# Optimization experiments

Measured on AMD Instinct MI355X. Metric: run time of the kernel, lower is better.

## Reference

```python
import jax, jax.numpy as jnp
import numpy as np

B, T, M, F, H, O = 64, 168, 256, 32, 128, 32
TWO_OVER_PI = 2.0 / np.pi


def setup_inputs() -> dict:
    key = jax.random.key(0)
    ks = jax.random.split(key, 8)
    return {
        "x": jax.random.normal(ks[0], (B, T, M, F), dtype=jnp.float32),
        "assoc_W": jax.random.normal(ks[1], (F, M, M), dtype=jnp.float32) * (1.0 / np.sqrt(M)),
        "W_ih": jax.random.normal(ks[2], (4 * H, F), dtype=jnp.float32) * (1.0 / np.sqrt(F)),
        "W_hh": jax.random.normal(ks[3], (4 * H, H), dtype=jnp.float32) * (1.0 / np.sqrt(H)),
        "b_ih": jax.random.normal(ks[4], (4 * H,), dtype=jnp.float32) * 0.01,
        "b_hh": jax.random.normal(ks[5], (4 * H,), dtype=jnp.float32) * 0.01,
        "dense_W": jax.random.normal(ks[6], (O, H), dtype=jnp.float32) * (1.0 / np.sqrt(H)),
        "dense_b": jax.random.normal(ks[7], (O,), dtype=jnp.float32) * 0.01,
    }


def _forward(x, assoc_W, W_ih, W_hh, b_ih, b_hh, dense_W, dense_b):
    # x: [B, T, M, F] (batch_first) -> scan over time
    xt = jnp.transpose(x, (1, 0, 2, 3))  # [T, B, M, F]
    b, m = x.shape[0], x.shape[2]
    h0 = jnp.zeros((b, m, H), dtype=x.dtype)
    c0 = jnp.zeros((b, m, H), dtype=x.dtype)

    def step(carry, xin):
        h, c = carry
        # ArcTanNorm: squash into (-1, 1)
        y = jnp.arctan(xin) * TWO_OVER_PI                      # [B, M, F]
        # ICFA: per-attribute association across map units
        y = jnp.einsum('amn,bna->bma', assoc_W, y)             # [B, M, F]
        # LSTM cell (shared weights across map units), PyTorch gate order i,f,g,o
        gates = (jnp.einsum('bmf,gf->bmg', y, W_ih) + b_ih
                 + jnp.einsum('bmh,gh->bmg', h, W_hh) + b_hh)  # [B, M, 4H]
        i, f, g, o = jnp.split(gates, 4, axis=-1)
        i, f, o = jax.nn.sigmoid(i), jax.nn.sigmoid(f), jax.nn.sigmoid(o)
        g = jnp.tanh(g)
        c = f * c + i * g
        h = o * jnp.tanh(c)
        # Dense output head
        out = jnp.einsum('bmh,oh->bmo', h, dense_W) + dense_b  # [B, M, O]
        return (h, c), out

    _, outs = jax.lax.scan(step, (h0, c0), xt)                 # [T, B, M, O]
    return jnp.transpose(outs, (1, 0, 2, 3))                   # [B, T, M, O]


def reference(x, assoc_W, W_ih, W_hh, b_ih, b_hh, dense_W, dense_b):
    return _forward(x, assoc_W, W_ih, W_hh, b_ih, b_hh, dense_W, dense_b)
```

## Files before the change

kernel.cpp:

```cpp
#include <hip/hip_runtime.h>

#define B_  64
#define T_  168
#define M_  256
#define F_  32
#define H_  128
#define O_  32
#define BT_ (B_*T_)

typedef __attribute__((ext_vector_type(8))) short bh8;
typedef __attribute__((ext_vector_type(4))) short sh4;
typedef __attribute__((ext_vector_type(4))) float fx4;

static __device__ __forceinline__ short f2bf(float f) {
  unsigned u = __float_as_uint(f);
  u += 0x7FFFu + ((u >> 16) & 1u);
  return (short)(u >> 16);
}
static __device__ __forceinline__ unsigned cvtpk(float lo, float hi) {
  unsigned r;
  asm("v_cvt_pk_bf16_f32 %0, %1, %2" : "=v"(r) : "v"(lo), "v"(hi));
  return r;
}
static __device__ __forceinline__ float ex2_(float x) {
#if __has_builtin(__builtin_amdgcn_exp2f)
  return __builtin_amdgcn_exp2f(x);
#else
  return exp2f(x);
#endif
}
static __device__ __forceinline__ float rcp_(float x) {
#if __has_builtin(__builtin_amdgcn_rcpf)
  return __builtin_amdgcn_rcpf(x);
#else
  return 1.0f / x;
#endif
}
static __device__ __forceinline__ float sigm(float x) {
  return 1.0f / (1.0f + __expf(-x));
}
static __device__ __forceinline__ float tanh_f(float x) {
  return 1.0f - 2.0f / (1.0f + __expf(2.0f * x));
}
static __device__ __forceinline__ fx4 mm16(bh8 a, bh8 b, fx4 c) {
  return __builtin_amdgcn_mfma_f32_16x16x32_bf16(a, b, c, 0, 0, 0);
}
static __device__ __forceinline__ bh8 cvt8(fx4 p0, fx4 p1) {
  bh8 s;
  s[0] = f2bf(p0[0]); s[1] = f2bf(p0[1]); s[2] = f2bf(p0[2]); s[3] = f2bf(p0[3]);
  s[4] = f2bf(p1[0]); s[5] = f2bf(p1[1]); s[6] = f2bf(p1[2]); s[7] = f2bf(p1[3]);
  return s;
}


__global__ __launch_bounds__(512) void atan_tr(const float* __restrict__ x,
                                               short* __restrict__ ut) {
  __shared__ __align__(16) short tl[8 * 32 * 68];
  const int tid = threadIdx.x;
  const float c2p = 0.63661977236758134f;
  for (int it = 0; it < 21; ++it) {
    const int id = blockIdx.x + it * 256;
    const int bt0 = (id >> 2) * 8, n0 = (id & 3) * 64;
    if (it) __syncthreads();
#pragma unroll
    for (int i = 0; i < 8; ++i) {
      int idx = tid + i * 512;
      int aq = idx & 7, nl = (idx >> 3) & 63, btl = idx >> 9;
      const float* src = x + (long)(bt0 + btl) * 8192 + (n0 + nl) * 32 + aq * 4;
      fx4 v = *(const fx4*)src;
      int base = (btl * 32 + aq * 4) * 68 + nl;
#pragma unroll
      for (int k = 0; k < 4; ++k)
        tl[base + k * 68] = f2bf(atanf(v[k]) * c2p);
    }
    __syncthreads();
#pragma unroll
    for (int p = 0; p < 8; ++p) {
      int r = p * 32 + (tid >> 4);
      int a = r >> 3, btl = r & 7, nq = tid & 15;
      sh4 v = *(const sh4*)&tl[(btl * 32 + a) * 68 + nq * 4];
      *(sh4*)&ut[((long)a * BT_ + bt0 + btl) * 256 + n0 + nq * 4] = v;
    }
  }
}

__global__ __launch_bounds__(512) void icfa_gemm(const short* __restrict__ ut,
                                                 const float* __restrict__ aw,
                                                 short* __restrict__ y) {
  __shared__ __align__(16) short waf[8 * 8 * 64 * 8];
  __shared__ __align__(16) short ubf[64 * 256];
  const int tid = threadIdx.x;
  const int lane = tid & 63, w = tid >> 6, l15 = lane & 15, l4 = lane >> 4;
  const int a = blockIdx.x >> 3, s = blockIdx.x & 7;
  const long ua = (long)a * BT_;

  for (int mh = 0; mh < 2; ++mh) {
    __syncthreads();
    for (int i = 0; i < 8; ++i) {
      int idx = tid + i * 512;
      int ln = idx & 63, ks = (idx >> 6) & 7, mt = idx >> 9;
      const float* src = aw + a * 65536 + (mh * 128 + mt * 16 + (ln & 15)) * 256
                         + ks * 32 + (ln >> 4) * 8;
      *(bh8*)&waf[idx * 8] = cvt8(*(const fx4*)src, *(const fx4*)(src + 4));
    }
    __syncthreads();
    bh8 Af[8];
#pragma unroll
    for (int ks = 0; ks < 8; ++ks)
      Af[ks] = *(const bh8*)&waf[((w * 8 + ks) * 64 + lane) * 8];

    for (int tile = 0; tile < 21; ++tile) {
      const int bt0 = s * 1344 + tile * 64;
      __syncthreads();
#pragma unroll
      for (int i = 0; i < 4; ++i) {
        int idx = tid + i * 512;
        int row = idx >> 5, slot = idx & 31;
        bh8 v = *(const bh8*)&ut[(ua + bt0 + row) * 256 + slot * 8];
        int sb = (row * 512 + slot * 16) ^ ((row & 7) << 4);
        *(bh8*)&((char*)ubf)[sb] = v;
      }
      __syncthreads();
#pragma unroll
      for (int ct = 0; ct < 4; ++ct) {
        fx4 acc = {0.f, 0.f, 0.f, 0.f};
        const int btr = ct * 16 + l15;
#pragma unroll
        for (int ks = 0; ks < 8; ++ks) {
          int byo = (btr * 512 + ks * 64 + l4 * 16) ^ ((btr & 7) << 4);
          bh8 Bf = *(const bh8*)&((char*)ubf)[byo];
          acc = mm16(Af[ks], Bf, acc);
        }
        sh4 o;
        o[0] = f2bf(acc[0]); o[1] = f2bf(acc[1]);
        o[2] = f2bf(acc[2]); o[3] = f2bf(acc[3]);
        *(sh4*)&y[(ua + bt0 + btr) * 256 + mh * 128 + w * 16 + l4 * 4] = o;
      }
    }
  }
}

__global__ __launch_bounds__(512, 2) void lstm_fused8(
    const short* __restrict__ y,
    const float* __restrict__ Wih, const float* __restrict__ Whh,
    const float* __restrict__ bih, const float* __restrict__ bhh,
    const float* __restrict__ dW,  const float* __restrict__ db,
    float* __restrict__ out) {
  __shared__ __align__(16) short hx[8704];
  __shared__ __align__(16) short ytr[2048];
  const int tid = threadIdx.x;
  const int lane = tid & 63, wg = tid >> 6, l15 = lane & 15, l4 = lane >> 4;
  const int bidx = blockIdx.x >> 2, m0 = (blockIdx.x & 3) * 64;
  const float L2E = 1.4426950408889634f;

  for (int i = 0; i < 9; ++i) {
    int j = tid + i * 512;
    if (j < 4352) ((int*)hx)[j] = 0;
  }
  bh8 wrg[4][4];
#pragma unroll
  for (int g = 0; g < 4; ++g)
#pragma unroll
    for (int ks = 0; ks < 4; ++ks) {
      const float* src = Whh + ((g * 8 + wg) * 16 + l15) * 128 + ks * 32 + l4 * 8;
      wrg[g][ks] = cvt8(*(const fx4*)src, *(const fx4*)(src + 4));
    }

  bh8 wfih[4]; float nb[4][4];
#pragma unroll
  for (int gate = 0; gate < 4; ++gate) {
    int grow = (gate * 8 + wg) * 16;
    const float* src = Wih + (grow + l15) * 32 + l4 * 8;
    wfih[gate] = cvt8(*(const fx4*)src, *(const fx4*)(src + 4));
#pragma unroll
    for (int r = 0; r < 4; ++r) {
      int g = grow + l4 * 4 + r;
      float b = bih[g] + bhh[g];
      nb[gate][r] = (gate == 2) ? (2.0f * L2E * b) : (-L2E * b);
    }
  }
  bh8 df[4]; float dbv[4];
  const int oc = wg >> 2, mt_d = wg & 3;
#pragma unroll
  for (int ks = 0; ks < 4; ++ks) {
    const float* src = dW + (oc * 16 + l15) * 128 + ks * 32 + l4 * 8;
    df[ks] = cvt8(*(const fx4*)src, *(const fx4*)(src + 4));
  }
#pragma unroll
  for (int r = 0; r < 4; ++r) dbv[r] = db[oc * 16 + l4 * 4 + r];

  float cst[4][4];
#pragma unroll
  for (int mt = 0; mt < 4; ++mt)
#pragma unroll
    for (int r = 0; r < 4; ++r) cst[mt][r] = 0.f;

  char* hxc = (char*)hx;
  const int hrb = l15 * 272 + l4 * 16;
  const int hdb = (mt_d * 16 + l15) * 272 + l4 * 16;
  const int hwb = l15 * 272 + wg * 32 + l4 * 8;
  const int ar = tid >> 4, mq = tid & 15;
  const long yrow = (long)ar * BT_ + (long)bidx * T_;
  const int ytre = ((mq >> 2) * 64 + ((ar >> 3) << 4) + (mq & 3) * 4) * 8 + (ar & 7);
  const long obB = (long)bidx * T_ * 8192
                 + (long)(m0 + mt_d * 16 + l15) * 32 + oc * 16 + l4 * 4;

  sh4 ys = *(const sh4*)&y[(yrow + 0) * 256 + m0 + mq * 4];
#pragma unroll
  for (int j = 0; j < 4; ++j) ytr[ytre + j * 8] = ys[j];
  ys = *(const sh4*)&y[(yrow + 1) * 256 + m0 + mq * 4];
  __syncthreads();

  for (int t = 0; t < T_; ++t) {
    sh4 ysn = {0, 0, 0, 0};
    if (t + 2 < T_) ysn = *(const sh4*)&y[(yrow + t + 2) * 256 + m0 + mq * 4];
    fx4 acc[4][4];
    {
      bh8 yB[4];
#pragma unroll
      for (int mt = 0; mt < 4; ++mt)
        yB[mt] = *(const bh8*)&ytr[(mt * 64 + lane) * 8];
      fx4 Z = {0.f, 0.f, 0.f, 0.f};
#pragma unroll
      for (int g = 0; g < 4; ++g)
#pragma unroll
        for (int mt = 0; mt < 4; ++mt)
          acc[g][mt] = mm16(wfih[g], yB[mt], Z);
    }
#pragma unroll
    for (int ks = 0; ks < 4; ++ks) {
      bh8 hB[4];
#pragma unroll
      for (int mt = 0; mt < 4; ++mt)
        hB[mt] = *(const bh8*)(hxc + hrb + mt * 4352 + ks * 64);
#pragma unroll
      for (int g = 0; g < 4; ++g)
#pragma unroll
        for (int mt = 0; mt < 4; ++mt)
          acc[g][mt] = mm16(wrg[g][ks], hB[mt], acc[g][mt]);
    }
    if (t > 0) {
      fx4 A = {dbv[0], dbv[1], dbv[2], dbv[3]};
#pragma unroll
      for (int ks = 0; ks < 4; ++ks) {
        bh8 hd = *(const bh8*)(hxc + hdb + ks * 64);
        A = mm16(df[ks], hd, A);
      }
      *(fx4*)&out[obB + (long)(t - 1) * 8192] = A;
    }
    float hn[4][4];
#pragma unroll
    for (int mt = 0; mt < 4; ++mt)
#pragma unroll
      for (int r = 0; r < 4; ++r) {
        float iv = rcp_(1.f + ex2_(fmaf(acc[0][mt][r], -L2E, nb[0][r])));
        float fv = rcp_(1.f + ex2_(fmaf(acc[1][mt][r], -L2E, nb[1][r])));
        float ov = rcp_(1.f + ex2_(fmaf(acc[3][mt][r], -L2E, nb[3][r])));
        float gv = 1.f - 2.f * rcp_(1.f + ex2_(fmaf(acc[2][mt][r], 2.f * L2E, nb[2][r])));
        float cn = fv * cst[mt][r] + iv * gv;
        cst[mt][r] = cn;
        float th = 1.f - 2.f * rcp_(1.f + ex2_(cn * (2.f * L2E)));
        hn[mt][r] = ov * th;
      }
    __syncthreads();
#pragma unroll
    for (int mt = 0; mt < 4; ++mt) {
      unsigned p01 = cvtpk(hn[mt][0], hn[mt][1]);
      unsigned p23 = cvtpk(hn[mt][2], hn[mt][3]);
      *(unsigned long long*)(hxc + hwb + mt * 4352) =
          (((unsigned long long)p23) << 32) | p01;
    }
    if (t + 1 < T_) {
#pragma unroll
      for (int j = 0; j < 4; ++j) ytr[ytre + j * 8] = ys[j];
    }
    ys = ysn;
    __syncthreads();
  }
  {
    fx4 A = {dbv[0], dbv[1], dbv[2], dbv[3]};
#pragma unroll
    for (int ks = 0; ks < 4; ++ks) {
      bh8 hd = *(const bh8*)(hxc + hdb + ks * 64);
      A = mm16(df[ks], hd, A);
    }
    *(fx4*)&out[obB + (long)(T_ - 1) * 8192] = A;
  }
}


__global__ __launch_bounds__(512) void icfa_mfma(const float* __restrict__ x,
                                                 const float* __restrict__ aw,
                                                 float* __restrict__ y) {
  __shared__ short waf[8 * 8 * 64 * 8];
  __shared__ short ubf[64 * 264];
  const int tid = threadIdx.x;
  const int lane = tid & 63, w = tid >> 6, l15 = lane & 15, l4 = lane >> 4;
  const int a = blockIdx.x >> 3, s = blockIdx.x & 7;
  const float c2p = 0.63661977236758134f;

  for (int mh = 0; mh < 2; ++mh) {
    __syncthreads();
    for (int i = 0; i < 8; ++i) {
      int idx = tid + i * 512;
      int ln = idx & 63, ks = (idx >> 6) & 7, mt = idx >> 9;
      const float* src = aw + a * 65536 + (mh * 128 + mt * 16 + (ln & 15)) * 256
                         + ks * 32 + (ln >> 4) * 8;
      *(bh8*)&waf[idx * 8] = cvt8(*(const fx4*)src, *(const fx4*)(src + 4));
    }
    __syncthreads();
    bh8 Af[8];
#pragma unroll
    for (int ks = 0; ks < 8; ++ks)
      Af[ks] = *(const bh8*)&waf[((w * 8 + ks) * 64 + lane) * 8];

    for (int tile = 0; tile < 21; ++tile) {
      const int bt0 = s * 1344 + tile * 64;
      __syncthreads();
#pragma unroll 4
      for (int i = 0; i < 32; ++i) {
        int idx = tid + i * 512;
        int n = idx & 255, btc = idx >> 8;
        float v = x[(long)(bt0 + btc) * 8192 + n * 32 + a];
        ubf[btc * 264 + n] = f2bf(atanf(v) * c2p);
      }
      __syncthreads();
#pragma unroll
      for (int ct = 0; ct < 4; ++ct) {
        fx4 acc = {0.f, 0.f, 0.f, 0.f};
#pragma unroll
        for (int ks = 0; ks < 8; ++ks) {
          bh8 Bf = *(const bh8*)&ubf[(ct * 16 + l15) * 264 + ks * 32 + l4 * 8];
          acc = mm16(Af[ks], Bf, acc);
        }
        long ybase = (long)(bt0 + ct * 16 + l15) * 8192
                     + (mh * 128 + w * 16 + l4 * 4) * 32 + a;
#pragma unroll
        for (int r = 0; r < 4; ++r) y[ybase + (long)r * 32] = acc[r];
      }
    }
  }
}

__global__ __launch_bounds__(512) void lstm_fused(
    const float* __restrict__ Wih, const float* __restrict__ Whh,
    const float* __restrict__ bih, const float* __restrict__ bhh,
    const float* __restrict__ dW,  const float* __restrict__ db,
    float* __restrict__ yo) {
  __shared__ short whf[32 * 4 * 64 * 8];
  __shared__ short hbuf[4 * 4 * 64 * 8];
  __shared__ short ytr[4 * 64 * 8];
  __shared__ float obuf[64 * 36];
  const int tid = threadIdx.x;
  const int lane = tid & 63, w = tid >> 6, l15 = lane & 15, l4 = lane >> 4;
  const int bidx = blockIdx.x >> 2, m0 = (blockIdx.x & 3) * 64;

  for (int i = 0; i < 16; ++i) {
    int idx = tid + i * 512;
    int ln = idx & 63, ks = (idx >> 6) & 3, ct = idx >> 8;
    const float* src = Whh + (ct * 16 + (ln & 15)) * 128 + ks * 32 + (ln >> 4) * 8;
    *(bh8*)&whf[idx * 8] = cvt8(*(const fx4*)src, *(const fx4*)(src + 4));
  }
  for (int i = 0; i < 8; ++i) ((int*)hbuf)[tid + i * 512] = 0;

  bh8 wfih[4]; float bias[4];
#pragma unroll
  for (int gate = 0; gate < 4; ++gate) {
    int g = (gate * 8 + w) * 16 + l15;
    bias[gate] = bih[g] + bhh[g];
    const float* src = Wih + g * 32 + l4 * 8;
    wfih[gate] = cvt8(*(const fx4*)src, *(const fx4*)(src + 4));
  }
  bh8 df[4];
  const int rtd = w >> 1, oc = w & 1;
  const int od = oc * 16 + l15;
  const float dbias = db[od];
#pragma unroll
  for (int ks = 0; ks < 4; ++ks) {
    const float* src = dW + od * 128 + ks * 32 + l4 * 8;
    df[ks] = cvt8(*(const fx4*)src, *(const fx4*)(src + 4));
  }

  float cst[4][4];
#pragma unroll
  for (int rt = 0; rt < 4; ++rt)
#pragma unroll
    for (int r = 0; r < 4; ++r) cst[rt][r] = 0.f;

  const int mloc = tid >> 3, a0 = (tid & 7) * 4;
  const long tb0 = (long)bidx * T_ * 8192;
  const long pfoff = (long)(m0 + mloc) * 32 + a0;
  const int ytre = ((mloc >> 4) * 64 + ((a0 >> 3) << 4) + (mloc & 15)) * 8 + (a0 & 7);
  const int kse = w >> 1;
  const int lnhi = (((w & 1) * 2 + (l15 >> 3)) << 4);
  const int e0 = l15 & 7;

  fx4 y4 = *(const fx4*)&yo[tb0 + pfoff];
  {
    sh4 p; p[0] = f2bf(y4[0]); p[1] = f2bf(y4[1]); p[2] = f2bf(y4[2]); p[3] = f2bf(y4[3]);
    *(sh4*)&ytr[ytre] = p;
  }
  y4 = *(const fx4*)&yo[tb0 + 8192 + pfoff];
  __syncthreads();

  for (int t = 0; t < T_; ++t) {
    const long off = tb0 + (long)t * 8192;
    float hn[4][4];
    bh8 Ball[4][4];
#pragma unroll
    for (int gate = 0; gate < 4; ++gate)
#pragma unroll
      for (int ks = 0; ks < 4; ++ks)
        Ball[gate][ks] =
            *(const bh8*)&whf[((((gate * 8 + w) * 4) + ks) * 64 + lane) * 8];
#pragma unroll
    for (int rt = 0; rt < 4; ++rt) {
      bh8 ya = *(const bh8*)&ytr[(rt * 64 + lane) * 8];
      bh8 hA[4];
#pragma unroll
      for (int ks = 0; ks < 4; ++ks)
        hA[ks] = *(const bh8*)&hbuf[((rt * 4 + ks) * 64 + lane) * 8];
      fx4 acc[4];
#pragma unroll
      for (int gate = 0; gate < 4; ++gate) {
        fx4 A = {bias[gate], bias[gate], bias[gate], bias[gate]};
        A = mm16(ya, wfih[gate], A);
#pragma unroll
        for (int ks = 0; ks < 4; ++ks) A = mm16(hA[ks], Ball[gate][ks], A);
        acc[gate] = A;
      }
#pragma unroll
      for (int r = 0; r < 4; ++r) {
        float iv = sigm(acc[0][r]);
        float fv = sigm(acc[1][r]);
        float gv = tanh_f(acc[2][r]);
        float ov = sigm(acc[3][r]);
        float cn = fv * cst[rt][r] + iv * gv;
        cst[rt][r] = cn;
        hn[rt][r] = ov * tanh_f(cn);
      }
    }
    __syncthreads();
#pragma unroll
    for (int rt = 0; rt < 4; ++rt)
#pragma unroll
      for (int r = 0; r < 4; ++r)
        hbuf[((rt * 4 + kse) * 64 + lnhi + l4 * 4 + r) * 8 + e0] = f2bf(hn[rt][r]);
    if (t + 1 < T_) {
      sh4 p; p[0] = f2bf(y4[0]); p[1] = f2bf(y4[1]); p[2] = f2bf(y4[2]); p[3] = f2bf(y4[3]);
      *(sh4*)&ytr[ytre] = p;
    }
    if (t + 2 < T_) y4 = *(const fx4*)&yo[off + 2 * 8192 + pfoff];
    __syncthreads();
    {
      fx4 A = {dbias, dbias, dbias, dbias};
#pragma unroll
      for (int ks = 0; ks < 4; ++ks) {
        bh8 hA2 = *(const bh8*)&hbuf[((rtd * 4 + ks) * 64 + lane) * 8];
        A = mm16(hA2, df[ks], A);
      }
#pragma unroll
      for (int r = 0; r < 4; ++r)
        obuf[(rtd * 16 + l4 * 4 + r) * 36 + oc * 16 + l15] = A[r];
    }
    __syncthreads();
    {
      fx4 o4 = *(const fx4*)&obuf[mloc * 36 + a0];
      *(fx4*)&yo[off + pfoff] = o4;
    }
  }
}

extern "C" void kernel_launch(void* const* d_in, const int* in_sizes, int n_in,
                              void* d_out, int out_size, void* d_ws, size_t ws_size,
                              hipStream_t stream) {
  const float* x   = (const float*)d_in[0];
  const float* aw  = (const float*)d_in[1];
  const float* wih = (const float*)d_in[2];
  const float* whh = (const float*)d_in[3];
  const float* bih = (const float*)d_in[4];
  const float* bhh = (const float*)d_in[5];
  const float* dw  = (const float*)d_in[6];
  const float* db  = (const float*)d_in[7];
  float* out = (float*)d_out;

  const size_t PLANE = (size_t)32 * BT_ * 256;
  const size_t NEED  = 2 * PLANE * sizeof(short);
  if (d_ws && ws_size >= NEED) {
    short* u = (short*)d_ws;
    short* yv = u + PLANE;
    hipLaunchKernelGGL(atan_tr,   dim3(256), dim3(512), 0, stream, x, u);
    hipLaunchKernelGGL(icfa_gemm, dim3(256), dim3(512), 0, stream, u, aw, yv);
    hipLaunchKernelGGL(lstm_fused8, dim3(256), dim3(512), 0, stream,
                       yv, wih, whh, bih, bhh, dw, db, out);
  } else {
    hipLaunchKernelGGL(icfa_mfma, dim3(256), dim3(512), 0, stream, x, aw, out);
    hipLaunchKernelGGL(lstm_fused, dim3(256), dim3(512), 0, stream,
                       wih, whh, bih, bhh, dw, db, out);
  }
}
```

Measured before the change: 886.3 us.

## Split LSTM recurrence across twice as many blocks with 32 map units each

The fused LSTM kernel now handles 32 map units per block instead of 64, launching 512 blocks instead of 256, with halved shared memory and per-thread accumulators. It requests four resident blocks per CU. The goal is more parallelism and latency hiding for the sequential time loop, since only 256 blocks previously covered the GPU. The cost is duplicated per-block weight loading and per-step barriers over less work per step. Half the waves now sit idle during the dense output head.

```diff
diff --git a/kernel.cpp b/kernel.cpp
--- a/kernel.cpp
+++ b/kernel.cpp
@@ -140,22 +140,22 @@
   }
 }
 
-__global__ __launch_bounds__(512, 2) void lstm_fused8(
+__global__ __launch_bounds__(512, 4) void lstm_fused9(
     const short* __restrict__ y,
     const float* __restrict__ Wih, const float* __restrict__ Whh,
     const float* __restrict__ bih, const float* __restrict__ bhh,
     const float* __restrict__ dW,  const float* __restrict__ db,
     float* __restrict__ out) {
-  __shared__ __align__(16) short hx[8704];
-  __shared__ __align__(16) short ytr[2048];
+  __shared__ __align__(16) short hx[4352];
+  __shared__ __align__(16) short ytr[1024];
   const int tid = threadIdx.x;
   const int lane = tid & 63, wg = tid >> 6, l15 = lane & 15, l4 = lane >> 4;
-  const int bidx = blockIdx.x >> 2, m0 = (blockIdx.x & 3) * 64;
+  const int bidx = blockIdx.x >> 3, m0 = (blockIdx.x & 7) * 32;
   const float L2E = 1.4426950408889634f;
 
-  for (int i = 0; i < 9; ++i) {
+  for (int i = 0; i < 5; ++i) {
     int j = tid + i * 512;
-    if (j < 4352) ((int*)hx)[j] = 0;
+    if (j < 2176) ((int*)hx)[j] = 0;
   }
   bh8 wrg[4][4];
 #pragma unroll
@@ -180,7 +180,7 @@
     }
   }
   bh8 df[4]; float dbv[4];
-  const int oc = wg >> 2, mt_d = wg & 3;
+  const int mt_d = wg & 1, oc = (wg >> 1) & 1;
 #pragma unroll
   for (int ks = 0; ks < 4; ++ks) {
     const float* src = dW + (oc * 16 + l15) * 128 + ks * 32 + l4 * 8;
@@ -189,9 +189,9 @@
 #pragma unroll
   for (int r = 0; r < 4; ++r) dbv[r] = db[oc * 16 + l4 * 4 + r];
 
-  float cst[4][4];
-#pragma unroll
-  for (int mt = 0; mt < 4; ++mt)
+  float cst[2][4];
+#pragma unroll
+  for (int mt = 0; mt < 2; ++mt)
 #pragma unroll
     for (int r = 0; r < 4; ++r) cst[mt][r] = 0.f;
 
@@ -199,47 +199,49 @@
   const int hrb = l15 * 272 + l4 * 16;
   const int hdb = (mt_d * 16 + l15) * 272 + l4 * 16;
   const int hwb = l15 * 272 + wg * 32 + l4 * 8;
-  const int ar = tid >> 4, mq = tid & 15;
+  const int ar = tid >> 4, mp = tid & 15;
   const long yrow = (long)ar * BT_ + (long)bidx * T_;
-  const int ytre = ((mq >> 2) * 64 + ((ar >> 3) << 4) + (mq & 3) * 4) * 8 + (ar & 7);
+  const int ml0 = mp * 2;
+  const int R0 = (ml0 >> 4) * 64 + ((ar >> 3) << 4) + (ml0 & 15);
+  const int ytre0 = R0 * 8 + (ar & 7);
   const long obB = (long)bidx * T_ * 8192
                  + (long)(m0 + mt_d * 16 + l15) * 32 + oc * 16 + l4 * 4;
 
-  sh4 ys = *(const sh4*)&y[(yrow + 0) * 256 + m0 + mq * 4];
-#pragma unroll
-  for (int j = 0; j < 4; ++j) ytr[ytre + j * 8] = ys[j];
-  ys = *(const sh4*)&y[(yrow + 1) * 256 + m0 + mq * 4];
+  int ys = *(const int*)&y[(yrow + 0) * 256 + m0 + mp * 2];
+  ytr[ytre0]     = (short)(ys & 0xffff);
+  ytr[ytre0 + 8] = (short)(((unsigned)ys) >> 16);
+  ys = *(const int*)&y[(yrow + 1) * 256 + m0 + mp * 2];
   __syncthreads();
 
   for (int t = 0; t < T_; ++t) {
-    sh4 ysn = {0, 0, 0, 0};
-    if (t + 2 < T_) ysn = *(const sh4*)&y[(yrow + t + 2) * 256 + m0 + mq * 4];
-    fx4 acc[4][4];
+    int ysn = 0;
+    if (t + 2 < T_) ysn = *(const int*)&y[(yrow + t + 2) * 256 + m0 + mp * 2];
+    fx4 acc[4][2];
     {
-      bh8 yB[4];
-#pragma unroll
-      for (int mt = 0; mt < 4; ++mt)
+      bh8 yB[2];
+#pragma unroll
+      for (int mt = 0; mt < 2; ++mt)
         yB[mt] = *(const bh8*)&ytr[(mt * 64 + lane) * 8];
       fx4 Z = {0.f, 0.f, 0.f, 0.f};
 #pragma unroll
       for (int g = 0; g < 4; ++g)
 #pragma unroll
-        for (int mt = 0; mt < 4; ++mt)
+        for (int mt = 0; mt < 2; ++mt)
           acc[g][mt] = mm16(wfih[g], yB[mt], Z);
     }
 #pragma unroll
     for (int ks = 0; ks < 4; ++ks) {
-      bh8 hB[4];
-#pragma unroll
-      for (int mt = 0; mt < 4; ++mt)
+      bh8 hB[2];
+#pragma unroll
+      for (int mt = 0; mt < 2; ++mt)
         hB[mt] = *(const bh8*)(hxc + hrb + mt * 4352 + ks * 64);
 #pragma unroll
       for (int g = 0; g < 4; ++g)
 #pragma unroll
-        for (int mt = 0; mt < 4; ++mt)
+        for (int mt = 0; mt < 2; ++mt)
           acc[g][mt] = mm16(wrg[g][ks], hB[mt], acc[g][mt]);
     }
-    if (t > 0) {
+    if (wg < 4 && t > 0) {
       fx4 A = {dbv[0], dbv[1], dbv[2], dbv[3]};
 #pragma unroll
       for (int ks = 0; ks < 4; ++ks) {
@@ -248,9 +250,9 @@
       }
       *(fx4*)&out[obB + (long)(t - 1) * 8192] = A;
     }
-    float hn[4][4];
-#pragma unroll
-    for (int mt = 0; mt < 4; ++mt)
+    float hn[2][4];
+#pragma unroll
+    for (int mt = 0; mt < 2; ++mt)
 #pragma unroll
       for (int r = 0; r < 4; ++r) {
         float iv = rcp_(1.f + ex2_(fmaf(acc[0][mt][r], -L2E, nb[0][r])));
@@ -264,20 +266,20 @@
       }
     __syncthreads();
 #pragma unroll
-    for (int mt = 0; mt < 4; ++mt) {
+    for (int mt = 0; mt < 2; ++mt) {
       unsigned p01 = cvtpk(hn[mt][0], hn[mt][1]);
       unsigned p23 = cvtpk(hn[mt][2], hn[mt][3]);
       *(unsigned long long*)(hxc + hwb + mt * 4352) =
           (((unsigned long long)p23) << 32) | p01;
     }
     if (t + 1 < T_) {
-#pragma unroll
-      for (int j = 0; j < 4; ++j) ytr[ytre + j * 8] = ys[j];
+      ytr[ytre0]     = (short)(ys & 0xffff);
+      ytr[ytre0 + 8] = (short)(((unsigned)ys) >> 16);
     }
     ys = ysn;
     __syncthreads();
   }
-  {
+  if (wg < 4) {
     fx4 A = {dbv[0], dbv[1], dbv[2], dbv[3]};
 #pragma unroll
     for (int ks = 0; ks < 4; ++ks) {
@@ -491,7 +493,7 @@
     short* yv = u + PLANE;
     hipLaunchKernelGGL(atan_tr,   dim3(256), dim3(512), 0, stream, x, u);
     hipLaunchKernelGGL(icfa_gemm, dim3(256), dim3(512), 0, stream, u, aw, yv);
-    hipLaunchKernelGGL(lstm_fused8, dim3(256), dim3(512), 0, stream,
+    hipLaunchKernelGGL(lstm_fused9, dim3(512), dim3(512), 0, stream,
                        yv, wih, whh, bih, bhh, dw, db, out);
   } else {
     hipLaunchKernelGGL(icfa_mfma, dim3(256), dim3(512), 0, stream, x, aw, out);
```

After: 1.770 ms. +99.7%, slower.
